# Kernel tuning notes

Measured on AMD Instinct MI355X. Metric: run time of the kernel, lower is better.

The kernel has to match this reference:

```python
import jax, jax.numpy as jnp
import numpy as np


def setup_inputs() -> dict:
    key = jax.random.key(0)
    k1, k2, k3, k4 = jax.random.split(key, 4)
    B, N, IN_DIM, QK_DIM = 8, 2048, 10, 32
    s = jax.random.normal(k1, (B, N, IN_DIM), dtype=jnp.float32)
    G = jax.random.uniform(k2, (B, N, N), dtype=jnp.float32)
    Wq = jax.random.normal(k3, (QK_DIM, IN_DIM), dtype=jnp.float32) * (1.0 / np.sqrt(IN_DIM))
    Wk = jax.random.normal(k4, (QK_DIM, IN_DIM), dtype=jnp.float32) * (1.0 / np.sqrt(IN_DIM))
    return {"s": s, "G": G, "Wq": Wq, "Wk": Wk}


def reference(s, G, Wq, Wk):
    # q, k: [B, N, qk_dim]  (nn.Linear with no bias: x @ W^T)
    q = jnp.einsum("bnd,qd->bnq", s, Wq)
    k = jnp.einsum("bnd,qd->bnq", s, Wk)
    # logits: [B, N, N]
    logits = jnp.einsum("bnq,bmq->bnm", q, k)
    w = jnp.square(logits) * G
    w = w / (jnp.sum(w, axis=-1, keepdims=True) + 1e-06)
    return w
```

## Files before the change

kernel.cpp:

```cpp
#include <hip/hip_runtime.h>
#include <stdint.h>

#define BB 8
#define NN 2048
#define IND 10
#define QK 32

__global__ __launch_bounds__(256) void qk_kernel(
    const float* __restrict__ s,
    const float* __restrict__ Wq, const float* __restrict__ Wk,
    float* __restrict__ q_ws, float* __restrict__ kt_ws) {
  int t = blockIdx.x * 256 + threadIdx.x;
  int b  = t >> 16;
  int n  = (t >> 5) & (NN - 1);
  int qd = t & 31;
  const float* srow = s + (size_t)(b * NN + n) * IND;
  float acq = 0.f, ack = 0.f;
#pragma unroll
  for (int d = 0; d < IND; ++d) {
    float sv = srow[d];
    acq = fmaf(sv, Wq[qd * IND + d], acq);
    ack = fmaf(sv, Wk[qd * IND + d], ack);
  }
  q_ws[(size_t)(b * NN + n) * QK + qd] = acq;
  int w  = n >> 9;
  int m  = n & 511;
  int i  = (m & 255) >> 2;
  int jc = ((m < 256) ? 0 : 4) + (m & 3);
  int ev = qd >> 2, c = qd & 3;
  kt_ws[(((size_t)(b * 4 + w) * 4096) + (ev * 8 + jc) * 64 + i) * 4 + c] = ack;
}

__global__ __launch_bounds__(256) void attn_kernel(
    const float* __restrict__ G,
    const float* __restrict__ q_ws, const float* __restrict__ kt_ws,
    float* __restrict__ out) {
  const int tid = threadIdx.x;
  const int b = blockIdx.y;
  const int r0 = blockIdx.x * 8;
  const int w = tid >> 6, lane = tid & 63;

  __shared__ float q_lds[4][256];
  __shared__ float red[4][8];

  {
    const float* qb = q_ws + ((size_t)b * NN + r0) * QK;
    *(float4*)&q_lds[w][4 * lane] = *(const float4*)&qb[4 * lane];
  }

  float acc[8][8];
#pragma unroll
  for (int r = 0; r < 8; ++r)
#pragma unroll
    for (int j = 0; j < 8; ++j) acc[r][j] = 0.f;

  const float4* kt =
      (const float4*)kt_ws + (size_t)(b * 4 + w) * 4096 + lane;

#pragma unroll
  for (int ev = 0; ev < 8; ++ev) {
    float q4[8][4];
#pragma unroll
    for (int r = 0; r < 8; ++r)
      *(float4*)q4[r] = *(const float4*)&q_lds[w][r * 32 + ev * 4];
#pragma unroll
    for (int j = 0; j < 8; ++j) {
      float4 k4 = kt[(ev * 8 + j) * 64];
#pragma unroll
      for (int r = 0; r < 8; ++r) {
        acc[r][j] = fmaf(q4[r][0], k4.x, acc[r][j]);
        acc[r][j] = fmaf(q4[r][1], k4.y, acc[r][j]);
        acc[r][j] = fmaf(q4[r][2], k4.z, acc[r][j]);
        acc[r][j] = fmaf(q4[r][3], k4.w, acc[r][j]);
      }
    }
  }

  const float* gb = G + ((size_t)b * NN + r0) * NN + 512 * w + 4 * lane;
  float rsum[8];
#pragma unroll
  for (int r = 0; r < 8; ++r) {
    float gg[8];
    *(float4*)&gg[0] = *(const float4*)(gb + (size_t)r * NN);
    *(float4*)&gg[4] = *(const float4*)(gb + (size_t)r * NN + 256);
    float sum = 0.f;
#pragma unroll
    for (int j = 0; j < 8; ++j) {
      float v = acc[r][j];
      v = v * v * gg[j];
      acc[r][j] = v;
      sum += v;
    }
#pragma unroll
    for (int off = 32; off >= 1; off >>= 1) sum += __shfl_xor(sum, off, 64);
    rsum[r] = sum;
  }

  if ((tid & 63) == 0) {
#pragma unroll
    for (int r = 0; r < 8; ++r) red[w][r] = rsum[r];
  }
  __syncthreads();

  float inv[8];
#pragma unroll
  for (int r = 0; r < 8; ++r) {
    float total = red[0][r] + red[1][r] + red[2][r] + red[3][r];
    inv[r] = 1.0f / (total + 1e-6f);
  }

  float* ob = out + ((size_t)b * NN + r0) * NN + 512 * w + 4 * lane;
#pragma unroll
  for (int r = 0; r < 8; ++r) {
    float4 o0, o1;
    o0.x = acc[r][0] * inv[r]; o0.y = acc[r][1] * inv[r];
    o0.z = acc[r][2] * inv[r]; o0.w = acc[r][3] * inv[r];
    o1.x = acc[r][4] * inv[r]; o1.y = acc[r][5] * inv[r];
    o1.z = acc[r][6] * inv[r]; o1.w = acc[r][7] * inv[r];
    *(float4*)(ob + (size_t)r * NN)       = o0;
    *(float4*)(ob + (size_t)r * NN + 256) = o1;
  }
}

extern "C" void kernel_launch(void* const* d_in, const int* in_sizes, int n_in,
                              void* d_out, int out_size, void* d_ws, size_t ws_size,
                              hipStream_t stream) {
  const float* s  = (const float*)d_in[0];
  const float* G  = (const float*)d_in[1];
  const float* Wq = (const float*)d_in[2];
  const float* Wk = (const float*)d_in[3];
  float* out = (float*)d_out;

  float* q_ws  = (float*)d_ws;
  float* kt_ws = q_ws + (size_t)BB * NN * QK;

  qk_kernel<<<(BB * NN * QK) / 256, 256, 0, stream>>>(s, Wq, Wk, q_ws, kt_ws);

  dim3 grid(NN / 8, BB);
  attn_kernel<<<grid, 256, 0, stream>>>(G, q_ws, kt_ws, out);
}
```

Before: 71.61 us.

## Prefetch G rows into LDS via async global_load_lds, double-buffered with compute

Issues direct global-to-LDS loads of G tiles before the QK dot-product loop, so G fetch latency overlaps with the logits compute. Rows are streamed through a two-slot LDS buffer, with vmcnt waits and sched barriers controlling when each pair of rows is consumed. This adds 32KB of LDS per block, which may reduce occupancy. The waitcnt bookkeeping also relies on the kt global loads finishing in order. There is no wave-level barrier, which is fine only because each wave reads back only its own LDS region.

```diff
diff --git a/kernel.cpp b/kernel.cpp
--- a/kernel.cpp
+++ b/kernel.cpp
@@ -31,6 +31,15 @@
   kt_ws[(((size_t)(b * 4 + w) * 4096) + (ev * 8 + jc) * 64 + i) * 4 + c] = ack;
 }
 
+__device__ __forceinline__ void gload_lds16(const float* src, float* lds_dst) {
+  __builtin_amdgcn_global_load_lds(
+      reinterpret_cast<const __attribute__((address_space(1))) uint32_t*>(
+          reinterpret_cast<uintptr_t>(src)),
+      reinterpret_cast<__attribute__((address_space(3))) uint32_t*>(
+          reinterpret_cast<uintptr_t>(lds_dst)),
+      16, 0, 0);
+}
+
 __global__ __launch_bounds__(256) void attn_kernel(
     const float* __restrict__ G,
     const float* __restrict__ q_ws, const float* __restrict__ kt_ws,
@@ -40,6 +49,7 @@
   const int r0 = blockIdx.x * 8;
   const int w = tid >> 6, lane = tid & 63;
 
+  __shared__ float g_buf[2][2][4][512];
   __shared__ float q_lds[4][256];
   __shared__ float red[4][8];
 
@@ -48,14 +58,27 @@
     *(float4*)&q_lds[w][4 * lane] = *(const float4*)&qb[4 * lane];
   }
 
+  const float4* kt =
+      (const float4*)kt_ws + (size_t)(b * 4 + w) * 4096 + lane;
+  const float* gb = G + ((size_t)b * NN + r0) * NN + 512 * w + 4 * lane;
+
+#pragma unroll
+  for (int cr = 0; cr < 2; ++cr)
+#pragma unroll
+    for (int h = 0; h < 2; ++h)
+      gload_lds16(gb + (size_t)cr * NN + 256 * h, &g_buf[0][cr][w][256 * h]);
+#pragma unroll
+  for (int cr = 0; cr < 2; ++cr)
+#pragma unroll
+    for (int h = 0; h < 2; ++h)
+      gload_lds16(gb + (size_t)(2 + cr) * NN + 256 * h,
+                  &g_buf[1][cr][w][256 * h]);
+
   float acc[8][8];
 #pragma unroll
   for (int r = 0; r < 8; ++r)
 #pragma unroll
     for (int j = 0; j < 8; ++j) acc[r][j] = 0.f;
-
-  const float4* kt =
-      (const float4*)kt_ws + (size_t)(b * 4 + w) * 4096 + lane;
 
 #pragma unroll
   for (int ev = 0; ev < 8; ++ev) {
@@ -76,25 +99,59 @@
     }
   }
 
-  const float* gb = G + ((size_t)b * NN + r0) * NN + 512 * w + 4 * lane;
   float rsum[8];
+
+#define PROCESS_ROW(rr, bi, cr)                                          \
+  {                                                                      \
+    float gg[8];                                                         \
+    *(float4*)&gg[0] = *(const float4*)&g_buf[bi][cr][w][4 * lane];      \
+    *(float4*)&gg[4] = *(const float4*)&g_buf[bi][cr][w][256 + 4 * lane];\
+    float sum = 0.f;                                                     \
+    _Pragma("unroll")                                                    \
+    for (int j = 0; j < 8; ++j) {                                        \
+      float v = acc[rr][j];                                              \
+      v = v * v * gg[j];                                                 \
+      acc[rr][j] = v;                                                    \
+      sum += v;                                                          \
+    }                                                                    \
+    _Pragma("unroll")                                                    \
+    for (int off = 32; off >= 1; off >>= 1)                              \
+      sum += __shfl_xor(sum, off, 64);                                   \
+    rsum[rr] = sum;                                                      \
+  }
+
+  asm volatile("s_waitcnt vmcnt(4)" ::: "memory");
+  __builtin_amdgcn_sched_barrier(0);
+  PROCESS_ROW(0, 0, 0)
+  PROCESS_ROW(1, 0, 1)
 #pragma unroll
-  for (int r = 0; r < 8; ++r) {
-    float gg[8];
-    *(float4*)&gg[0] = *(const float4*)(gb + (size_t)r * NN);
-    *(float4*)&gg[4] = *(const float4*)(gb + (size_t)r * NN + 256);
-    float sum = 0.f;
+  for (int cr = 0; cr < 2; ++cr)
 #pragma unroll
-    for (int j = 0; j < 8; ++j) {
-      float v = acc[r][j];
-      v = v * v * gg[j];
-      acc[r][j] = v;
-      sum += v;
-    }
+    for (int h = 0; h < 2; ++h)
+      gload_lds16(gb + (size_t)(4 + cr) * NN + 256 * h,
+                  &g_buf[0][cr][w][256 * h]);
+
+  asm volatile("s_waitcnt vmcnt(4)" ::: "memory");
+  __builtin_amdgcn_sched_barrier(0);
+  PROCESS_ROW(2, 1, 0)
+  PROCESS_ROW(3, 1, 1)
 #pragma unroll
-    for (int off = 32; off >= 1; off >>= 1) sum += __shfl_xor(sum, off, 64);
-    rsum[r] = sum;
-  }
+  for (int cr = 0; cr < 2; ++cr)
+#pragma unroll
+    for (int h = 0; h < 2; ++h)
+      gload_lds16(gb + (size_t)(6 + cr) * NN + 256 * h,
+                  &g_buf[1][cr][w][256 * h]);
+
+  asm volatile("s_waitcnt vmcnt(4)" ::: "memory");
+  __builtin_amdgcn_sched_barrier(0);
+  PROCESS_ROW(4, 0, 0)
+  PROCESS_ROW(5, 0, 1)
+
+  asm volatile("s_waitcnt vmcnt(0)" ::: "memory");
+  __builtin_amdgcn_sched_barrier(0);
+  PROCESS_ROW(6, 1, 0)
+  PROCESS_ROW(7, 1, 1)
+#undef PROCESS_ROW
 
   if ((tid & 63) == 0) {
 #pragma unroll
```

New measurement: 93.64 us. +30.8%, slower.
